# Kernel optimization log

Measured on AMD Instinct MI355X. Metric: run time of the kernel, lower is better.

## Reference

```python
import jax, jax.numpy as jnp
import numpy as np


def gcn_conv(h, src, dst, n, W, b):
    # PyG GCNConv: linear, add self-loops, symmetric norm, scatter-sum, bias
    h = h @ W
    loop = jnp.arange(n)
    s = jnp.concatenate([src, loop])
    d = jnp.concatenate([dst, loop])
    deg = jax.ops.segment_sum(jnp.ones_like(d, h.dtype), d, num_segments=n)
    dinv = jnp.where(deg > 0, jax.lax.rsqrt(deg), 0.0)
    norm = dinv[s] * dinv[d]  # [E+N]
    out = jax.ops.segment_sum(h[s] * norm[:, None], d, num_segments=n)
    return out + b


def setup_inputs() -> dict:
    key = jax.random.key(0)
    ks = jax.random.split(key, 4)
    N, E, F_IN, F_H, F_OUT = 10000, 320000, 512, 128, 40
    x = jax.random.normal(ks[0], (N, F_IN), dtype=jnp.float32)
    edge_index = jax.random.randint(ks[1], (2, E), 0, N, dtype=jnp.int64)
    W1 = jax.random.normal(ks[2], (F_IN, F_H), dtype=jnp.float32) * (1.0 / np.sqrt(F_IN))
    b1 = jnp.zeros((F_H,), jnp.float32)
    W2 = jax.random.normal(ks[3], (F_H, F_OUT), dtype=jnp.float32) * (1.0 / np.sqrt(F_H))
    b2 = jnp.zeros((F_OUT,), jnp.float32)
    return {"x": x, "edge_index": edge_index, "W1": W1, "b1": b1, "W2": W2, "b2": b2}


def reference(x, edge_index, W1, b1, W2, b2):
    n = x.shape[0]
    src, dst = edge_index[0], edge_index[1]
    h = jax.nn.relu(gcn_conv(x, src, dst, n, W1, b1))
    logits = gcn_conv(h, src, dst, n, W2, b2)
    # regularizer: dense adjacency from edge list (duplicates summed), trace(L @ L)
    A = jnp.zeros((n, n), jnp.float32).at[src, dst].add(1.0)
    reg_loss = jnp.sum(A * A.T)  # == trace(A @ A)
    return jax.nn.log_softmax(logits, axis=1), reg_loss
```

## Files before the change

### kernel.cpp

```cpp
#include <hip/hip_runtime.h>
#include <hip/hip_bf16.h>


#define CAP 128

typedef __attribute__((ext_vector_type(8))) short short8;
typedef __attribute__((ext_vector_type(4))) float float4v;

__device__ __forceinline__ unsigned short f2bf(float f) {
    __hip_bfloat16 b = __float2bfloat16(f);
    return *reinterpret_cast<unsigned short*>(&b);
}
__device__ __forceinline__ float bf2f(unsigned short u) {
    __hip_bfloat16 b = *reinterpret_cast<__hip_bfloat16*>(&u);
    return __bfloat162float(b);
}

__global__ void k_prep(const float* __restrict__ x, unsigned short* __restrict__ xh, int total4,
                       const float* __restrict__ W1, unsigned short* __restrict__ Bh1,
                       unsigned short* __restrict__ Bl1,
                       const float* __restrict__ W2, unsigned short* __restrict__ Bh2,
                       unsigned short* __restrict__ Bl2,
                       int* __restrict__ zbase, int zints,
                       int convB, int p1B, int p2B) {
    int b = blockIdx.x;
    if (b < convB) {
        int i = b * 256 + threadIdx.x;
        if (i < total4) {
            float4 v = ((const float4*)x)[i];
            ushort4 h;
            h.x = f2bf(v.x); h.y = f2bf(v.y); h.z = f2bf(v.z); h.w = f2bf(v.w);
            ((ushort4*)xh)[i] = h;
        }
        return;
    }
    b -= convB;
    if (b < p1B) {
        int t = b * 256 + threadIdx.x;
        int lane = t & 63;
        int f = (t >> 6) % 8;
        int kb = (t >> 6) / 8;
        int kbase = kb * 32 + (lane >> 4) * 8;
        int n = f * 16 + (lane & 15);
        unsigned short hj[8], lj[8];
#pragma unroll
        for (int j = 0; j < 8; j++) {
            float v = W1[(size_t)(kbase + j) * 128 + n];
            unsigned short hb = f2bf(v);
            hj[j] = hb;
            lj[j] = f2bf(v - bf2f(hb));
        }
        ushort4 h0 = {hj[0], hj[1], hj[2], hj[3]}, h1 = {hj[4], hj[5], hj[6], hj[7]};
        ushort4 l0 = {lj[0], lj[1], lj[2], lj[3]}, l1 = {lj[4], lj[5], lj[6], lj[7]};
        ((ushort4*)Bh1)[t * 2] = h0; ((ushort4*)Bh1)[t * 2 + 1] = h1;
        ((ushort4*)Bl1)[t * 2] = l0; ((ushort4*)Bl1)[t * 2 + 1] = l1;
        return;
    }
    b -= p1B;
    if (b < p2B) {
        int t = b * 256 + threadIdx.x;
        if (t >= 4 * 3 * 64) return;
        int lane = t & 63;
        int f = (t >> 6) % 3;
        int kb = (t >> 6) / 3;
        int kbase = kb * 32 + (lane >> 4) * 8;
        int n = f * 16 + (lane & 15);
        unsigned short hj[8], lj[8];
#pragma unroll
        for (int j = 0; j < 8; j++) {
            float v = (n < 40) ? W2[(size_t)(kbase + j) * 40 + n] : 0.f;
            unsigned short hb = f2bf(v);
            hj[j] = hb;
            lj[j] = f2bf(v - bf2f(hb));
        }
        ushort4 h0 = {hj[0], hj[1], hj[2], hj[3]}, h1 = {hj[4], hj[5], hj[6], hj[7]};
        ushort4 l0 = {lj[0], lj[1], lj[2], lj[3]}, l1 = {lj[4], lj[5], lj[6], lj[7]};
        ((ushort4*)Bh2)[t * 2] = h0; ((ushort4*)Bh2)[t * 2 + 1] = h1;
        ((ushort4*)Bl2)[t * 2] = l0; ((ushort4*)Bl2)[t * 2 + 1] = l1;
        return;
    }
    b -= p2B;
    {
        int i = b * 256 + threadIdx.x;
        if (i < zints) zbase[i] = 0;
    }
}

template <int NF, int KB>
__global__ void k_gemm1_fill(const unsigned short* __restrict__ Xh,
                             const unsigned short* __restrict__ Bh,
                             const unsigned short* __restrict__ Bl,
                             unsigned short* __restrict__ H0, int M,
                             const int* __restrict__ src, const int* __restrict__ dst, int E,
                             int* __restrict__ cnt, unsigned short* __restrict__ csr,
                             int gemmBlocks) {
    if ((int)blockIdx.x >= gemmBlocks) {
        int e = ((int)blockIdx.x - gemmBlocks) * 128 + (int)threadIdx.x;
        if (e >= E) return;
        int d = dst[e];
        int pos = atomicAdd(&cnt[d], 1);
        if (pos < CAP) csr[(size_t)d * CAP + pos] = (unsigned short)src[e];
        return;
    }
    const int K = KB * 32, N = NF * 16;
    const int CH = NF * 64;
    __shared__ uint4 sB[2][2 * NF * 64];
    int w = threadIdx.x >> 6, lane = threadIdx.x & 63;
    int m0 = blockIdx.x * 32 + w * 16;
    bool valid = (m0 < M);
    int arow = valid ? (m0 + (lane & 15)) : 0;

    const uint4* GH = (const uint4*)Bh;
    const uint4* GL = (const uint4*)Bl;
    float4v acc[NF] = {};
    const short8* A = (const short8*)(Xh + (size_t)arow * K) + (lane >> 4);
    short8 a = A[0];

#pragma unroll
    for (int c = threadIdx.x; c < CH; c += 128) {
        sB[0][c] = GH[c];
        sB[0][CH + c] = GL[c];
    }
    __syncthreads();

    for (int kb = 0; kb < KB; kb++) {
        int slot = kb & 1;
        if (kb + 1 < KB) {
            const uint4* gh = GH + (kb + 1) * CH;
            const uint4* gl = GL + (kb + 1) * CH;
#pragma unroll
            for (int c = threadIdx.x; c < CH; c += 128) {
                sB[slot ^ 1][c] = gh[c];
                sB[slot ^ 1][CH + c] = gl[c];
            }
        }
        short8 an = (kb + 1 < KB) ? A[(kb + 1) * 4] : a;
        const short8* sb = (const short8*)sB[slot];
#pragma unroll
        for (int f = 0; f < NF; f++) {
            short8 bh = sb[f * 64 + lane];
            short8 bl = sb[CH + f * 64 + lane];
            acc[f] = __builtin_amdgcn_mfma_f32_16x16x32_bf16(a, bh, acc[f], 0, 0, 0);
            acc[f] = __builtin_amdgcn_mfma_f32_16x16x32_bf16(a, bl, acc[f], 0, 0, 0);
        }
        a = an;
        __syncthreads();
    }
    if (!valid) return;
    int row = (lane >> 4) * 4, col = lane & 15;
#pragma unroll
    for (int f = 0; f < NF; f++)
#pragma unroll
        for (int r = 0; r < 4; r++)
            H0[(size_t)(m0 + row + r) * N + f * 16 + col] = f2bf(acc[f][r]);
}

template <int NF, int KB>
__global__ void k_mfma_gemm2(const unsigned short* __restrict__ Ab,
                             const unsigned short* __restrict__ Bh,
                             const unsigned short* __restrict__ Bl,
                             unsigned short* __restrict__ LGb, int M) {
    const int K = KB * 32, N = NF * 16;
    const int TOT = KB * NF * 64;
    __shared__ uint4 sB[2 * KB * NF * 64];
#pragma unroll
    for (int c = threadIdx.x; c < TOT; c += 256) {
        sB[c] = ((const uint4*)Bh)[c];
        sB[TOT + c] = ((const uint4*)Bl)[c];
    }
    __syncthreads();
    int w = threadIdx.x >> 6, lane = threadIdx.x & 63;
    int m0 = blockIdx.x * 64 + w * 16;
    if (m0 >= M) return;
    float4v acc[NF] = {};
    const short8* A = (const short8*)(Ab + (size_t)(m0 + (lane & 15)) * K) + (lane >> 4);
    const short8* sb = (const short8*)sB;
#pragma unroll
    for (int kb = 0; kb < KB; kb++) {
        short8 a = A[kb * 4];
#pragma unroll
        for (int f = 0; f < NF; f++) {
            short8 bh = sb[(kb * NF + f) * 64 + lane];
            short8 bl = sb[TOT + (kb * NF + f) * 64 + lane];
            acc[f] = __builtin_amdgcn_mfma_f32_16x16x32_bf16(a, bh, acc[f], 0, 0, 0);
            acc[f] = __builtin_amdgcn_mfma_f32_16x16x32_bf16(a, bl, acc[f], 0, 0, 0);
        }
    }
    int row = (lane >> 4) * 4, col = lane & 15;
#pragma unroll
    for (int f = 0; f < NF; f++)
#pragma unroll
        for (int r = 0; r < 4; r++)
            LGb[(size_t)(m0 + row + r) * N + f * 16 + col] = f2bf(acc[f][r]);
}

__global__ void k_agg1_reg(const int* __restrict__ cnt, const unsigned short* __restrict__ csr,
                           const unsigned short* __restrict__ H, const float* __restrict__ b1,
                           unsigned* __restrict__ aggb,
                           const int* __restrict__ src, const int* __restrict__ dst, int E,
                           float* __restrict__ regp, int Nn, int aggBlocks) {
    if ((int)blockIdx.x < aggBlocks) {
        int wid = blockIdx.x * 4 + (threadIdx.x >> 6);
        int lane = threadIdx.x & 63;
        if (wid >= Nn) return;
        int len = min(cnt[wid], CAP);
        float dd = rsqrtf((float)len + 1.0f);
        const unsigned* H2 = (const unsigned*)H;
        unsigned ph = H2[(size_t)wid * 64 + lane];
        float sw = dd * dd;
        float accx = bf2f((unsigned short)(ph & 0xffff)) * sw;
        float accy = bf2f((unsigned short)(ph >> 16)) * sw;
        const unsigned short* row = csr + (size_t)wid * CAP;
        int j = 0;
        for (; j + 16 <= len; j += 16) {
            uint4 iv0 = *(const uint4*)(row + j);
            uint4 iv1 = *(const uint4*)(row + j + 8);
            int s[16];
            s[0] = iv0.x & 0xffff; s[1] = iv0.x >> 16; s[2] = iv0.y & 0xffff; s[3] = iv0.y >> 16;
            s[4] = iv0.z & 0xffff; s[5] = iv0.z >> 16; s[6] = iv0.w & 0xffff; s[7] = iv0.w >> 16;
            s[8] = iv1.x & 0xffff; s[9] = iv1.x >> 16; s[10] = iv1.y & 0xffff; s[11] = iv1.y >> 16;
            s[12] = iv1.z & 0xffff; s[13] = iv1.z >> 16; s[14] = iv1.w & 0xffff; s[15] = iv1.w >> 16;
            int cn[16];
            unsigned p[16];
#pragma unroll
            for (int q = 0; q < 16; q++) cn[q] = cnt[s[q]];
#pragma unroll
            for (int q = 0; q < 16; q++) p[q] = H2[(size_t)s[q] * 64 + lane];
#pragma unroll
            for (int q = 0; q < 16; q++) {
                float wq = rsqrtf((float)min(cn[q], CAP) + 1.0f) * dd;
                accx += wq * bf2f((unsigned short)(p[q] & 0xffff));
                accy += wq * bf2f((unsigned short)(p[q] >> 16));
            }
        }
        for (; j + 8 <= len; j += 8) {
            uint4 iv0 = *(const uint4*)(row + j);
            int s[8];
            s[0] = iv0.x & 0xffff; s[1] = iv0.x >> 16; s[2] = iv0.y & 0xffff; s[3] = iv0.y >> 16;
            s[4] = iv0.z & 0xffff; s[5] = iv0.z >> 16; s[6] = iv0.w & 0xffff; s[7] = iv0.w >> 16;
            int cn[8];
            unsigned p[8];
#pragma unroll
            for (int q = 0; q < 8; q++) cn[q] = cnt[s[q]];
#pragma unroll
            for (int q = 0; q < 8; q++) p[q] = H2[(size_t)s[q] * 64 + lane];
#pragma unroll
            for (int q = 0; q < 8; q++) {
                float wq = rsqrtf((float)min(cn[q], CAP) + 1.0f) * dd;
                accx += wq * bf2f((unsigned short)(p[q] & 0xffff));
                accy += wq * bf2f((unsigned short)(p[q] >> 16));
            }
        }
        for (; j < len; j++) {
            int s0 = row[j];
            float w0 = rsqrtf((float)min(cnt[s0], CAP) + 1.0f) * dd;
            unsigned p0 = H2[(size_t)s0 * 64 + lane];
            accx += w0 * bf2f((unsigned short)(p0 & 0xffff));
            accy += w0 * bf2f((unsigned short)(p0 >> 16));
        }
        float2 bb = ((const float2*)b1)[lane];
        float vx = accx + bb.x, vy = accy + bb.y;
        vx = vx > 0.f ? vx : 0.f;
        vy = vy > 0.f ? vy : 0.f;
        aggb[(size_t)wid * 64 + lane] = (unsigned)f2bf(vx) | ((unsigned)f2bf(vy) << 16);
    } else {
        int e = ((int)blockIdx.x - aggBlocks) * 256 + (int)threadIdx.x;
        int c = 0;
        if (e < E) {
            int s = src[e];
            unsigned d = (unsigned)dst[e];
            int len = min(cnt[s], CAP);
            const unsigned short* row = csr + (size_t)s * CAP;
            for (int i = 0; i < len; i += 8) {
                uint4 v = *(const uint4*)(row + i);
                c += ((v.x & 0xffffu) == d) ? 1 : 0;
                c += ((v.x >> 16) == d && i + 1 < len) ? 1 : 0;
                c += ((v.y & 0xffffu) == d && i + 2 < len) ? 1 : 0;
                c += ((v.y >> 16) == d && i + 3 < len) ? 1 : 0;
                c += ((v.z & 0xffffu) == d && i + 4 < len) ? 1 : 0;
                c += ((v.z >> 16) == d && i + 5 < len) ? 1 : 0;
                c += ((v.w & 0xffffu) == d && i + 6 < len) ? 1 : 0;
                c += ((v.w >> 16) == d && i + 7 < len) ? 1 : 0;
            }
        }
#pragma unroll
        for (int off = 32; off; off >>= 1) c += __shfl_xor(c, off, 64);
        if ((threadIdx.x & 63) == 0 && c) atomicAdd(regp, (float)c);
    }
}

__global__ void k_agg2_lsm(const int* __restrict__ cnt, const unsigned short* __restrict__ csr,
                           const unsigned short* __restrict__ LGb, const float* __restrict__ b2,
                           const float* __restrict__ regp, float* __restrict__ out,
                           int Nn, int F) {
    int wid = (blockIdx.x * blockDim.x + threadIdx.x) >> 6;
    int lane = threadIdx.x & 63;
    if (wid >= Nn) return;
    int len = min(cnt[wid], CAP);
    float dd = rsqrtf((float)len + 1.0f);
    bool act = lane < F;
    float acc = act ? bf2f(LGb[(size_t)wid * 48 + lane]) * dd * dd : 0.f;
    const unsigned short* row = csr + (size_t)wid * CAP;
    int j = 0;
    for (; j + 8 <= len; j += 8) {
        uint4 idv = *(const uint4*)(row + j);
        int s[8];
        s[0] = idv.x & 0xffff; s[1] = idv.x >> 16; s[2] = idv.y & 0xffff; s[3] = idv.y >> 16;
        s[4] = idv.z & 0xffff; s[5] = idv.z >> 16; s[6] = idv.w & 0xffff; s[7] = idv.w >> 16;
        int cn[8];
        float a[8];
#pragma unroll
        for (int q = 0; q < 8; q++) cn[q] = cnt[s[q]];
#pragma unroll
        for (int q = 0; q < 8; q++) a[q] = act ? bf2f(LGb[(size_t)s[q] * 48 + lane]) : 0.f;
#pragma unroll
        for (int q = 0; q < 8; q++) {
            float wq = rsqrtf((float)min(cn[q], CAP) + 1.0f) * dd;
            acc += wq * a[q];
        }
    }
    for (; j < len; j++) {
        int s0 = row[j];
        float w0 = rsqrtf((float)min(cnt[s0], CAP) + 1.0f) * dd;
        float a0 = act ? bf2f(LGb[(size_t)s0 * 48 + lane]) : 0.f;
        acc += w0 * a0;
    }
    float v = act ? acc + b2[lane] : -1e30f;
    float m = v;
#pragma unroll
    for (int off = 32; off; off >>= 1) m = fmaxf(m, __shfl_xor(m, off, 64));
    float ex = act ? expf(v - m) : 0.f;
    float ssum = ex;
#pragma unroll
    for (int off = 32; off; off >>= 1) ssum += __shfl_xor(ssum, off, 64);
    if (act) out[(size_t)wid * F + lane] = v - m - logf(ssum);
    if (wid == 0 && lane == 0) out[(size_t)Nn * F] = regp[0];
}

extern "C" void kernel_launch(void* const* d_in, const int* in_sizes, int n_in,
                              void* d_out, int out_size, void* d_ws, size_t ws_size,
                              hipStream_t stream) {
    const float* x  = (const float*)d_in[0];
    const int*   ei = (const int*)d_in[1];
    const float* W1 = (const float*)d_in[2];
    const float* b1 = (const float*)d_in[3];
    const float* W2 = (const float*)d_in[4];
    const float* b2 = (const float*)d_in[5];
    float* out = (float*)d_out;

    const int FH   = in_sizes[3];
    const int FOUT = in_sizes[5];
    const int FIN  = in_sizes[2] / FH;
    const int Nn   = in_sizes[0] / FIN;
    const int E    = in_sizes[1] / 2;
    const int* src = ei;
    const int* dst = ei + E;

    int*   cnt  = (int*)d_ws;
    float* regp = (float*)(cnt + Nn);
    unsigned short* csr   = (unsigned short*)(regp + 16);
    unsigned short* Xh    = csr + (size_t)Nn * CAP;
    unsigned short* H0b   = Xh + (size_t)Nn * FIN;
    unsigned short* AGG1b = H0b + (size_t)Nn * FH;
    unsigned short* Bh1   = AGG1b + (size_t)Nn * FH;
    unsigned short* Bl1   = Bh1 + 65536;
    unsigned short* Bh2   = Bl1 + 65536;
    unsigned short* Bl2   = Bh2 + 6144;
    unsigned short* LGb   = Bl2 + 6144;

    int total4 = Nn * FIN / 4;
    int convB = (total4 + 255) / 256;
    int p1B = (16 * 8 * 64) / 256;
    int p2B = (4 * 3 * 64 + 255) / 256;
    int zints = Nn + 16;
    int zB = (zints + 255) / 256;
    k_prep<<<convB + p1B + p2B + zB, 256, 0, stream>>>(
        x, Xh, total4, W1, Bh1, Bl1, W2, Bh2, Bl2, cnt, zints, convB, p1B, p2B);

    int gemmB = (Nn + 31) / 32;
    int fillB = (E + 127) / 128;
    k_gemm1_fill<8, 16><<<gemmB + fillB, 128, 0, stream>>>(
        Xh, Bh1, Bl1, H0b, Nn, src, dst, E, cnt, csr, gemmB);

    int aggBlocks = (Nn + 3) / 4;
    int regBlocks = (E + 255) / 256;
    k_agg1_reg<<<aggBlocks + regBlocks, 256, 0, stream>>>(
        cnt, csr, H0b, b1, (unsigned*)AGG1b, src, dst, E, regp, Nn, aggBlocks);

    k_mfma_gemm2<3, 4><<<(Nn + 63) / 64, 256, 0, stream>>>(AGG1b, Bh2, Bl2, LGb, Nn);

    k_agg2_lsm<<<(Nn * 64 + 255) / 256, 256, 0, stream>>>(
        cnt, csr, LGb, b2, regp, out, Nn, FOUT);
}
```

Before: 188.6 us.

## Fold source-side degree scaling into GEMM epilogues and drop per-edge count gathers

The source-node normalization dinv[s] is now applied once per row in the epilogue of each GEMM, so the aggregation kernels only sum pre-scaled neighbor rows and apply dinv[d] once at the end. This removes the per-edge gather of cnt and the rsqrt from both aggregation loops. To make counts available to GEMM1, the x-to-bf16 conversion and CSR fill move into a separate kernel that runs before GEMM1, giving up the earlier overlap of the fill with GEMM1. Index arithmetic is also switched to 32-bit, and bf16 values are unpacked with shifts.

```diff
diff --git a/kernel.cpp b/kernel.cpp
--- a/kernel.cpp
+++ b/kernel.cpp
@@ -16,25 +16,12 @@
     return __bfloat162float(b);
 }
 
-__global__ void k_prep(const float* __restrict__ x, unsigned short* __restrict__ xh, int total4,
-                       const float* __restrict__ W1, unsigned short* __restrict__ Bh1,
+__global__ void k_prep(const float* __restrict__ W1, unsigned short* __restrict__ Bh1,
                        unsigned short* __restrict__ Bl1,
                        const float* __restrict__ W2, unsigned short* __restrict__ Bh2,
                        unsigned short* __restrict__ Bl2,
-                       int* __restrict__ zbase, int zints,
-                       int convB, int p1B, int p2B) {
+                       int* __restrict__ zbase, int zints, int p1B, int p2B) {
     int b = blockIdx.x;
-    if (b < convB) {
-        int i = b * 256 + threadIdx.x;
-        if (i < total4) {
-            float4 v = ((const float4*)x)[i];
-            ushort4 h;
-            h.x = f2bf(v.x); h.y = f2bf(v.y); h.z = f2bf(v.z); h.w = f2bf(v.w);
-            ((ushort4*)xh)[i] = h;
-        }
-        return;
-    }
-    b -= convB;
     if (b < p1B) {
         int t = b * 256 + threadIdx.x;
         int lane = t & 63;
@@ -86,22 +73,34 @@
     }
 }
 
+__global__ void k_conv_fill(const float* __restrict__ x, unsigned short* __restrict__ xh,
+                            int total4,
+                            const int* __restrict__ src, const int* __restrict__ dst, int E,
+                            int* __restrict__ cnt, unsigned short* __restrict__ csr,
+                            int convB) {
+    if ((int)blockIdx.x < convB) {
+        int i = blockIdx.x * 256 + threadIdx.x;
+        if (i < total4) {
+            float4 v = ((const float4*)x)[i];
+            ushort4 h;
+            h.x = f2bf(v.x); h.y = f2bf(v.y); h.z = f2bf(v.z); h.w = f2bf(v.w);
+            ((ushort4*)xh)[i] = h;
+        }
+        return;
+    }
+    int e = ((int)blockIdx.x - convB) * 256 + (int)threadIdx.x;
+    if (e >= E) return;
+    int d = dst[e];
+    int pos = atomicAdd(&cnt[d], 1);
+    if (pos < CAP) csr[(size_t)d * CAP + pos] = (unsigned short)src[e];
+}
+
 template <int NF, int KB>
-__global__ void k_gemm1_fill(const unsigned short* __restrict__ Xh,
-                             const unsigned short* __restrict__ Bh,
-                             const unsigned short* __restrict__ Bl,
-                             unsigned short* __restrict__ H0, int M,
-                             const int* __restrict__ src, const int* __restrict__ dst, int E,
-                             int* __restrict__ cnt, unsigned short* __restrict__ csr,
-                             int gemmBlocks) {
-    if ((int)blockIdx.x >= gemmBlocks) {
-        int e = ((int)blockIdx.x - gemmBlocks) * 128 + (int)threadIdx.x;
-        if (e >= E) return;
-        int d = dst[e];
-        int pos = atomicAdd(&cnt[d], 1);
-        if (pos < CAP) csr[(size_t)d * CAP + pos] = (unsigned short)src[e];
-        return;
-    }
+__global__ void k_gemm1(const unsigned short* __restrict__ Xh,
+                        const unsigned short* __restrict__ Bh,
+                        const unsigned short* __restrict__ Bl,
+                        unsigned short* __restrict__ H0, int M,
+                        const int* __restrict__ cnt) {
     const int K = KB * 32, N = NF * 16;
     const int CH = NF * 64;
     __shared__ uint4 sB[2][2 * NF * 64];
@@ -148,18 +147,23 @@
     }
     if (!valid) return;
     int row = (lane >> 4) * 4, col = lane & 15;
+    float dd[4];
+#pragma unroll
+    for (int r = 0; r < 4; r++)
+        dd[r] = rsqrtf((float)min(cnt[m0 + row + r], CAP) + 1.0f);
 #pragma unroll
     for (int f = 0; f < NF; f++)
 #pragma unroll
         for (int r = 0; r < 4; r++)
-            H0[(size_t)(m0 + row + r) * N + f * 16 + col] = f2bf(acc[f][r]);
+            H0[(size_t)(m0 + row + r) * N + f * 16 + col] = f2bf(acc[f][r] * dd[r]);
 }
 
 template <int NF, int KB>
 __global__ void k_mfma_gemm2(const unsigned short* __restrict__ Ab,
                              const unsigned short* __restrict__ Bh,
                              const unsigned short* __restrict__ Bl,
-                             unsigned short* __restrict__ LGb, int M) {
+                             unsigned short* __restrict__ LGb, int M,
+                             const int* __restrict__ cnt) {
     const int K = KB * 32, N = NF * 16;
     const int TOT = KB * NF * 64;
     __shared__ uint4 sB[2 * KB * NF * 64];
@@ -187,11 +191,15 @@
         }
     }
     int row = (lane >> 4) * 4, col = lane & 15;
+    float dd[4];
+#pragma unroll
+    for (int r = 0; r < 4; r++)
+        dd[r] = rsqrtf((float)min(cnt[m0 + row + r], CAP) + 1.0f);
 #pragma unroll
     for (int f = 0; f < NF; f++)
 #pragma unroll
         for (int r = 0; r < 4; r++)
-            LGb[(size_t)(m0 + row + r) * N + f * 16 + col] = f2bf(acc[f][r]);
+            LGb[(size_t)(m0 + row + r) * N + f * 16 + col] = f2bf(acc[f][r] * dd[r]);
 }
 
 __global__ void k_agg1_reg(const int* __restrict__ cnt, const unsigned short* __restrict__ csr,
@@ -204,65 +212,54 @@
         int lane = threadIdx.x & 63;
         if (wid >= Nn) return;
         int len = min(cnt[wid], CAP);
-        float dd = rsqrtf((float)len + 1.0f);
         const unsigned* H2 = (const unsigned*)H;
-        unsigned ph = H2[(size_t)wid * 64 + lane];
-        float sw = dd * dd;
-        float accx = bf2f((unsigned short)(ph & 0xffff)) * sw;
-        float accy = bf2f((unsigned short)(ph >> 16)) * sw;
+        unsigned ph = H2[(unsigned)(wid << 6) + lane];
+        float accx = __uint_as_float(ph << 16);
+        float accy = __uint_as_float(ph & 0xffff0000u);
         const unsigned short* row = csr + (size_t)wid * CAP;
         int j = 0;
         for (; j + 16 <= len; j += 16) {
             uint4 iv0 = *(const uint4*)(row + j);
             uint4 iv1 = *(const uint4*)(row + j + 8);
-            int s[16];
+            unsigned s[16];
             s[0] = iv0.x & 0xffff; s[1] = iv0.x >> 16; s[2] = iv0.y & 0xffff; s[3] = iv0.y >> 16;
             s[4] = iv0.z & 0xffff; s[5] = iv0.z >> 16; s[6] = iv0.w & 0xffff; s[7] = iv0.w >> 16;
             s[8] = iv1.x & 0xffff; s[9] = iv1.x >> 16; s[10] = iv1.y & 0xffff; s[11] = iv1.y >> 16;
             s[12] = iv1.z & 0xffff; s[13] = iv1.z >> 16; s[14] = iv1.w & 0xffff; s[15] = iv1.w >> 16;
-            int cn[16];
             unsigned p[16];
 #pragma unroll
-            for (int q = 0; q < 16; q++) cn[q] = cnt[s[q]];
-#pragma unroll
-            for (int q = 0; q < 16; q++) p[q] = H2[(size_t)s[q] * 64 + lane];
+            for (int q = 0; q < 16; q++) p[q] = H2[(s[q] << 6) + lane];
 #pragma unroll
             for (int q = 0; q < 16; q++) {
-                float wq = rsqrtf((float)min(cn[q], CAP) + 1.0f) * dd;
-                accx += wq * bf2f((unsigned short)(p[q] & 0xffff));
-                accy += wq * bf2f((unsigned short)(p[q] >> 16));
+                accx += __uint_as_float(p[q] << 16);
+                accy += __uint_as_float(p[q] & 0xffff0000u);
             }
         }
         for (; j + 8 <= len; j += 8) {
             uint4 iv0 = *(const uint4*)(row + j);
-            int s[8];
+            unsigned s[8];
             s[0] = iv0.x & 0xffff; s[1] = iv0.x >> 16; s[2] = iv0.y & 0xffff; s[3] = iv0.y >> 16;
             s[4] = iv0.z & 0xffff; s[5] = iv0.z >> 16; s[6] = iv0.w & 0xffff; s[7] = iv0.w >> 16;
-            int cn[8];
             unsigned p[8];
 #pragma unroll
-            for (int q = 0; q < 8; q++) cn[q] = cnt[s[q]];
-#pragma unroll
-            for (int q = 0; q < 8; q++) p[q] = H2[(size_t)s[q] * 64 + lane];
+            for (int q = 0; q < 8; q++) p[q] = H2[(s[q] << 6) + lane];
 #pragma unroll
             for (int q = 0; q < 8; q++) {
-                float wq = rsqrtf((float)min(cn[q], CAP) + 1.0f) * dd;
-                accx += wq * bf2f((unsigned short)(p[q] & 0xffff));
-                accy += wq * bf2f((unsigned short)(p[q] >> 16));
+                accx += __uint_as_float(p[q] << 16);
+                accy += __uint_as_float(p[q] & 0xffff0000u);
             }
         }
         for (; j < len; j++) {
-            int s0 = row[j];
-            float w0 = rsqrtf((float)min(cnt[s0], CAP) + 1.0f) * dd;
-            unsigned p0 = H2[(size_t)s0 * 64 + lane];
-            accx += w0 * bf2f((unsigned short)(p0 & 0xffff));
-            accy += w0 * bf2f((unsigned short)(p0 >> 16));
-        }
+            unsigned p0 = H2[((unsigned)row[j] << 6) + lane];
+            accx += __uint_as_float(p0 << 16);
+            accy += __uint_as_float(p0 & 0xffff0000u);
+        }
+        float dd = rsqrtf((float)len + 1.0f);
         float2 bb = ((const float2*)b1)[lane];
-        float vx = accx + bb.x, vy = accy + bb.y;
+        float vx = dd * accx + bb.x, vy = dd * accy + bb.y;
         vx = vx > 0.f ? vx : 0.f;
         vy = vy > 0.f ? vy : 0.f;
-        aggb[(size_t)wid * 64 + lane] = (unsigned)f2bf(vx) | ((unsigned)f2bf(vy) << 16);
+        aggb[(unsigned)(wid << 6) + lane] = (unsigned)f2bf(vx) | ((unsigned)f2bf(vy) << 16);
     } else {
         int e = ((int)blockIdx.x - aggBlocks) * 256 + (int)threadIdx.x;
         int c = 0;
@@ -297,35 +294,28 @@
     int lane = threadIdx.x & 63;
     if (wid >= Nn) return;
     int len = min(cnt[wid], CAP);
-    float dd = rsqrtf((float)len + 1.0f);
     bool act = lane < F;
-    float acc = act ? bf2f(LGb[(size_t)wid * 48 + lane]) * dd * dd : 0.f;
+    unsigned base = (unsigned)wid * 48 + lane;
+    float acc = act ? bf2f(LGb[base]) : 0.f;
     const unsigned short* row = csr + (size_t)wid * CAP;
     int j = 0;
     for (; j + 8 <= len; j += 8) {
         uint4 idv = *(const uint4*)(row + j);
-        int s[8];
+        unsigned s[8];
         s[0] = idv.x & 0xffff; s[1] = idv.x >> 16; s[2] = idv.y & 0xffff; s[3] = idv.y >> 16;
         s[4] = idv.z & 0xffff; s[5] = idv.z >> 16; s[6] = idv.w & 0xffff; s[7] = idv.w >> 16;
-        int cn[8];
-        float a[8];
-#pragma unroll
-        for (int q = 0; q < 8; q++) cn[q] = cnt[s[q]];
-#pragma unroll
-        for (int q = 0; q < 8; q++) a[q] = act ? bf2f(LGb[(size_t)s[q] * 48 + lane]) : 0.f;
-#pragma unroll
-        for (int q = 0; q < 8; q++) {
-            float wq = rsqrtf((float)min(cn[q], CAP) + 1.0f) * dd;
-            acc += wq * a[q];
-        }
+        unsigned short a[8];
+#pragma unroll
+        for (int q = 0; q < 8; q++) a[q] = act ? LGb[s[q] * 48 + lane] : (unsigned short)0;
+#pragma unroll
+        for (int q = 0; q < 8; q++) acc += __uint_as_float((unsigned)a[q] << 16);
     }
     for (; j < len; j++) {
-        int s0 = row[j];
-        float w0 = rsqrtf((float)min(cnt[s0], CAP) + 1.0f) * dd;
-        float a0 = act ? bf2f(LGb[(size_t)s0 * 48 + lane]) : 0.f;
-        acc += w0 * a0;
-    }
-    float v = act ? acc + b2[lane] : -1e30f;
+        unsigned short a0 = act ? LGb[(unsigned)row[j] * 48 + lane] : (unsigned short)0;
+        acc += __uint_as_float((unsigned)a0 << 16);
+    }
+    float dd = rsqrtf((float)len + 1.0f);
+    float v = act ? dd * acc + b2[lane] : -1e30f;
     float m = v;
 #pragma unroll
     for (int off = 32; off; off >>= 1) m = fmaxf(m, __shfl_xor(m, off, 64));
@@ -368,26 +358,26 @@
     unsigned short* Bl2   = Bh2 + 6144;
     unsigned short* LGb   = Bl2 + 6144;
 
-    int total4 = Nn * FIN / 4;
-    int convB = (total4 + 255) / 256;
     int p1B = (16 * 8 * 64) / 256;
     int p2B = (4 * 3 * 64 + 255) / 256;
     int zints = Nn + 16;
     int zB = (zints + 255) / 256;
-    k_prep<<<convB + p1B + p2B + zB, 256, 0, stream>>>(
-        x, Xh, total4, W1, Bh1, Bl1, W2, Bh2, Bl2, cnt, zints, convB, p1B, p2B);
-
-    int gemmB = (Nn + 31) / 32;
-    int fillB = (E + 127) / 128;
-    k_gemm1_fill<8, 16><<<gemmB + fillB, 128, 0, stream>>>(
-        Xh, Bh1, Bl1, H0b, Nn, src, dst, E, cnt, csr, gemmB);
+    k_prep<<<p1B + p2B + zB, 256, 0, stream>>>(W1, Bh1, Bl1, W2, Bh2, Bl2,
+                                               cnt, zints, p1B, p2B);
+
+    int total4 = Nn * FIN / 4;
+    int convB = (total4 + 255) / 256;
+    int fillB = (E + 255) / 256;
+    k_conv_fill<<<convB + fillB, 256, 0, stream>>>(x, Xh, total4, src, dst, E, cnt, csr, convB);
+
+    k_gemm1<8, 16><<<(Nn + 31) / 32, 128, 0, stream>>>(Xh, Bh1, Bl1, H0b, Nn, cnt);
 
     int aggBlocks = (Nn + 3) / 4;
     int regBlocks = (E + 255) / 256;
     k_agg1_reg<<<aggBlocks + regBlocks, 256, 0, stream>>>(
         cnt, csr, H0b, b1, (unsigned*)AGG1b, src, dst, E, regp, Nn, aggBlocks);
 
-    k_mfma_gemm2<3, 4><<<(Nn + 63) / 64, 256, 0, stream>>>(AGG1b, Bh2, Bl2, LGb, Nn);
+    k_mfma_gemm2<3, 4><<<(Nn + 63) / 64, 256, 0, stream>>>(AGG1b, Bh2, Bl2, LGb, Nn, cnt);
 
     k_agg2_lsm<<<(Nn * 64 + 255) / 256, 256, 0, stream>>>(
         cnt, csr, LGb, b2, regp, out, Nn, FOUT);
```

Result: slower. 194.2 us (+3.0%).
